# Kernel optimization log

Measured on AMD Instinct MI355X. Metric: run time of the kernel, lower is better.

## Reference

```python
import jax, jax.numpy as jnp
import numpy as np

B, P, N, E = 32, 1024, 1024, 128
HQ = 128  # head_num * qkv_dim == embedding_dim
SQRT_E = 11.313708498984761
LOGIT_CLIP = 10.0


def setup_inputs() -> dict:
    key = jax.random.key(0)
    ks = jax.random.split(key, 16)
    s = 1.0 / np.sqrt(E)
    return {
        "encoded_nodes": jax.random.normal(ks[0], (B, N, E), jnp.float32),
        "encoded_q1": jax.random.normal(ks[1], (B, P, E), jnp.float32),
        "encoded_q2": jax.random.normal(ks[2], (B, P, E), jnp.float32),
        "encoded_last_node": jax.random.normal(ks[3], (B, P, E), jnp.float32),
        "load": jax.random.uniform(ks[4], (B, P), jnp.float32),
        "left": jax.random.uniform(ks[5], (B, P), jnp.float32),
        "cur_dist": jax.random.uniform(ks[6], (B, P, N), jnp.float32),
        "log_scale": jnp.ones((), jnp.float32),
        "ninf_mask": jnp.zeros((B, P, N), jnp.float32),
        "Wq1": jax.random.normal(ks[7], (E, HQ), jnp.float32) * s,
        "Wq2": jax.random.normal(ks[8], (E, HQ), jnp.float32) * s,
        "Wq_last": jax.random.normal(ks[9], (E + 2, HQ), jnp.float32) * s,
        "Wk": jax.random.normal(ks[10], (E, HQ), jnp.float32) * s,
        "Wv": jax.random.normal(ks[11], (E, HQ), jnp.float32) * s,
        "AFT_dist_alpha": jnp.ones((1,), jnp.float32),
        "probs_dist_alpha": jnp.ones((1,), jnp.float32),
    }


def reference(encoded_nodes, encoded_q1, encoded_q2, encoded_last_node, load, left,
              cur_dist, log_scale, ninf_mask, Wq1, Wq2, Wq_last, Wk, Wv,
              AFT_dist_alpha, probs_dist_alpha):
    # set_kv / set_q1 / set_q2
    k = encoded_nodes @ Wk                      # [B,N,HQ]
    v = encoded_nodes @ Wv                      # [B,N,HQ]
    single_head_key = jnp.swapaxes(encoded_nodes, 1, 2)  # [B,E,N]
    q1 = encoded_q1 @ Wq1                       # [B,P,HQ]
    q2 = encoded_q2 @ Wq2

    input_cat = jnp.concatenate([encoded_last_node, load[:, :, None], left[:, :, None]], axis=2)
    q_last = input_cat @ Wq_last                # [B,P,HQ]
    q = q1 + q2 + q_last

    cur_dist_out = -cur_dist                    # [B,P,N]
    sigmoid_q = jax.nn.sigmoid(q)
    bias_scale = log_scale * AFT_dist_alpha[0] * cur_dist_out + ninf_mask
    e_bias = jnp.exp(bias_scale)                # [B,P,N]
    ek = jnp.exp(k)                             # [B,N,HQ]
    num = jnp.nan_to_num(jnp.einsum('bpn,bnd->bpd', e_bias, ek * v))
    den = jnp.nan_to_num(jnp.einsum('bpn,bnd->bpd', e_bias, ek)) + 1e-20
    AFT_out = sigmoid_q * (num / den)           # [B,P,HQ]

    score = jnp.einsum('bpd,bdn->bpn', AFT_out, single_head_key)
    score_scaled = score / SQRT_E + log_scale * probs_dist_alpha[0] * cur_dist_out
    score_clipped = LOGIT_CLIP * jnp.tanh(score_scaled)
    probs = jax.nn.softmax(score_clipped + ninf_mask, axis=2)
    return probs
```

## Files before the change

### kernel.cpp

```cpp
#include <hip/hip_runtime.h>
#include <math.h>

#define Bb 32
#define Pp 1024
#define Nn 1024

typedef unsigned short u16;
typedef __bf16 bf16x8 __attribute__((ext_vector_type(8)));
typedef float f32x4 __attribute__((ext_vector_type(4)));
typedef u16 us8 __attribute__((ext_vector_type(8)));
typedef u16 us4 __attribute__((ext_vector_type(4)));

#define MFMA __builtin_amdgcn_mfma_f32_16x16x32_bf16

static constexpr float INV_SQRT_E = 0.08838834764831845f;

__device__ __forceinline__ bf16x8 asbf(us8 v) { return __builtin_bit_cast(bf16x8, v); }

__device__ __forceinline__ void bsplit(float x, u16& h, u16& l) {
  unsigned u = __float_as_uint(x);
  unsigned r = u + 0x7FFF + ((u >> 16) & 1);
  h = (u16)(r >> 16);
  float hf = __uint_as_float((unsigned)h << 16);
  float lof = x - hf;
  unsigned u2 = __float_as_uint(lof);
  unsigned r2 = u2 + 0x7FFF + ((u2 >> 16) & 1);
  l = (u16)(r2 >> 16);
}

__device__ __forceinline__ void tsplit(float x, u16& h, u16& l) {
  unsigned u = __float_as_uint(x);
  h = (u16)(u >> 16);
  float lof = x - __uint_as_float(u & 0xFFFF0000u);
  l = (u16)(__float_as_uint(lof) >> 16);
}

__device__ __forceinline__ float exp10tanh(float s) {
  float ax = fabsf(s);
  float u = __expf(-2.0f * ax);
  float r = __builtin_amdgcn_rcpf(1.0f + u);
  float tt = fmaf(-2.0f * u, r, 1.0f);
  tt = copysignf(tt, s);
  return __expf(10.0f * tt);
}

__global__ __launch_bounds__(256) void prep_weights(
    const float* __restrict__ Wq1, const float* __restrict__ Wq2,
    const float* __restrict__ Wql, const float* __restrict__ Wk,
    const float* __restrict__ Wv, u16* __restrict__ wcat_hi, u16* __restrict__ wcat_lo,
    u16* __restrict__ wkv_hi, u16* __restrict__ wkv_lo) {
  int t = threadIdx.x;
  if (blockIdx.x == 0) {
    for (int i = t; i < 128 * 384; i += 256) {
      int c = i / 384, k = i % 384;
      float v = (k < 128) ? Wq1[k * 128 + c]
                          : (k < 256) ? Wq2[(k - 128) * 128 + c] : Wql[(k - 256) * 128 + c];
      u16 h, l;
      bsplit(v, h, l);
      wcat_hi[i] = h;
      wcat_lo[i] = l;
    }
  } else {
    for (int i = t; i < 256 * 128; i += 256) {
      int c = i >> 7, k = i & 127;
      float v = (c < 128) ? Wk[k * 128 + c] : Wv[k * 128 + (c - 128)];
      u16 h, l;
      bsplit(v, h, l);
      wkv_hi[i] = h;
      wkv_lo[i] = l;
    }
  }
}

__global__ __launch_bounds__(256, 1) void kv_prep(
    const float* __restrict__ nodes, const u16* __restrict__ wkv_hi,
    const u16* __restrict__ wkv_lo, u16* __restrict__ ekkP_hi, u16* __restrict__ ekkP_lo,
    u16* __restrict__ nodesP_hi, u16* __restrict__ nodesP_lo) {
  __shared__ u16 a_hi[32 * 136], a_lo[32 * 136];
  __shared__ float kvbuf[32 * 264];
  const int t = threadIdx.x;
  const int xcd = blockIdx.x & 7, jj = blockIdx.x >> 3;
  const int b = xcd * 4 + (jj >> 5);
  const int n0 = (jj & 31) * 32;
  for (int i = t; i < 4096; i += 256) {
    int n = i >> 7, d = i & 127;
    float v = nodes[((long)(b * 1024 + n0 + n)) * 128 + d];
    u16 h, l;
    bsplit(v, h, l);
    a_hi[n * 136 + d] = h;
    a_lo[n * 136 + d] = l;
  }
  __syncthreads();
  const int lane = t & 63, w = t >> 6;
  const int lr = lane & 15, lg = lane >> 4;
  f32x4 acc0[2][4] = {}, acc1[2][4] = {};
#pragma unroll
  for (int ks = 0; ks < 4; ++ks) {
    us8 ah[2], al[2];
#pragma unroll
    for (int mt = 0; mt < 2; ++mt) {
      int ro = (lr + 16 * mt) * 136 + ks * 32 + lg * 8;
      ah[mt] = *(const us8*)&a_hi[ro];
      al[mt] = *(const us8*)&a_lo[ro];
    }
    us8 bh[4], bl[4];
#pragma unroll
    for (int cc = 0; cc < 4; ++cc) {
      long off = (long)((w * 4 + cc) * 16 + lr) * 128 + ks * 32 + lg * 8;
      bh[cc] = *(const us8*)&wkv_hi[off];
      bl[cc] = *(const us8*)&wkv_lo[off];
    }
#pragma unroll
    for (int mt = 0; mt < 2; ++mt)
#pragma unroll
      for (int cc = 0; cc < 4; ++cc) {
        acc0[mt][cc] = MFMA(asbf(ah[mt]), asbf(bh[cc]), acc0[mt][cc], 0, 0, 0);
        acc1[mt][cc] = MFMA(asbf(al[mt]), asbf(bh[cc]), acc1[mt][cc], 0, 0, 0);
        acc1[mt][cc] = MFMA(asbf(ah[mt]), asbf(bl[cc]), acc1[mt][cc], 0, 0, 0);
      }
  }
#pragma unroll
  for (int mt = 0; mt < 2; ++mt)
#pragma unroll
    for (int cc = 0; cc < 4; ++cc) {
      int c = (w * 4 + cc) * 16 + lr;
#pragma unroll
      for (int r = 0; r < 4; ++r)
        kvbuf[(lg * 4 + r + 16 * mt) * 264 + c] = acc0[mt][cc][r] + acc1[mt][cc][r];
    }
  __syncthreads();
#pragma unroll
  for (int jo = 0; jo < 4; ++jo) {
    int c = jo * 64 + (t & 63);
    int i4 = t >> 6;
    int kcol = (c < 128) ? c : (c - 128);
    us8 h8, l8;
#pragma unroll
    for (int jq = 0; jq < 8; ++jq) {
      int n = i4 * 8 + jq;
      float kv = kvbuf[n * 264 + kcol];
      float ek = __expf(kv);
      float val = (c < 128) ? ek * kvbuf[n * 264 + c + 128] : ek;
      u16 h, l;
      bsplit(val, h, l);
      h8[jq] = h;
      l8[jq] = l;
    }
    long o = (((long)b * 128 + (n0 >> 3) + i4) * 256 + c) * 8;
    *(us8*)&ekkP_hi[o] = h8;
    *(us8*)&ekkP_lo[o] = l8;
  }
  {
    int pl = t >> 7, r = t & 127;
    int dgrp = r >> 3, nb = r & 7;
    const u16* src = pl ? a_lo : a_hi;
    u16* dst = pl ? nodesP_lo : nodesP_hi;
#pragma unroll
    for (int i = 0; i < 4; ++i) {
      int n = nb + 8 * i;
      us8 v = *(const us8*)&src[n * 136 + dgrp * 8];
      *(us8*)&dst[(((long)(b * 16 + dgrp)) * 1024 + n0 + n) * 8] = v;
    }
  }
}

__global__ __launch_bounds__(256) void qsig_prep(
    const float* __restrict__ q1m, const float* __restrict__ q2m,
    const float* __restrict__ lnm, const float* __restrict__ loadv,
    const float* __restrict__ leftv, const float* __restrict__ Wql,
    const u16* __restrict__ wcat_hi, const u16* __restrict__ wcat_lo,
    float* __restrict__ qsig) {
  const int t = threadIdx.x;
  const int lane = t & 63, w = t >> 6;
  const int lr = lane & 15, lg = lane >> 4;
  const long p0 = (long)blockIdx.x * 16;
  const long arow = p0 + lr;
  f32x4 qacc[2] = {};
#pragma unroll 2
  for (int s = 0; s < 12; ++s) {
    const float* __restrict__ src = (s < 4) ? q1m : (s < 8) ? q2m : lnm;
    long ao = arow * 128 + (s & 3) * 32 + lg * 8;
    float4 a0 = *(const float4*)&src[ao];
    float4 a1 = *(const float4*)&src[ao + 4];
    float av[8] = {a0.x, a0.y, a0.z, a0.w, a1.x, a1.y, a1.z, a1.w};
    us8 ah, al;
#pragma unroll
    for (int jq = 0; jq < 8; ++jq) {
      u16 hh, ll;
      tsplit(av[jq], hh, ll);
      ah[jq] = hh;
      al[jq] = ll;
    }
#pragma unroll
    for (int cf = 0; cf < 2; ++cf) {
      int c = w * 32 + cf * 16 + lr;
      us8 bh = *(const us8*)&wcat_hi[c * 384 + s * 32 + lg * 8];
      us8 bl = *(const us8*)&wcat_lo[c * 384 + s * 32 + lg * 8];
      qacc[cf] = MFMA(asbf(ah), asbf(bh), qacc[cf], 0, 0, 0);
      qacc[cf] = MFMA(asbf(al), asbf(bh), qacc[cf], 0, 0, 0);
      qacc[cf] = MFMA(asbf(ah), asbf(bl), qacc[cf], 0, 0, 0);
    }
  }
#pragma unroll
  for (int cf = 0; cf < 2; ++cf) {
    int c = w * 32 + cf * 16 + lr;
    float wl1 = Wql[128 * 128 + c], wl2 = Wql[129 * 128 + c];
#pragma unroll
    for (int r = 0; r < 4; ++r) {
      int row = lg * 4 + r;
      float qv = qacc[cf][r] + loadv[p0 + row] * wl1 + leftv[p0 + row] * wl2;
      qsig[(p0 + row) * 128 + c] = 1.0f / (1.0f + __expf(-qv));
    }
  }
}

struct DFset {
  float4 d0, d1, f0, f1;
};

__global__ __launch_bounds__(512, 2) void ndaft_gemm(
    const float* __restrict__ cdist, const float* __restrict__ ninf,
    const u16* __restrict__ ekkP_hi, const u16* __restrict__ ekkP_lo,
    const float* __restrict__ qsig, u16* __restrict__ aftP_hi,
    u16* __restrict__ aftP_lo, u16* __restrict__ bias16,
    const float* __restrict__ logs, const float* __restrict__ aal,
    const float* __restrict__ pal) {
  __shared__ u16 lds[2][8704];
  const int t = threadIdx.x;
  const int lane = t & 63, w = t >> 6;
  const int lr = lane & 15, lg = lane >> 4;
  const int wr = w >> 2, wc = w & 3;
  const int xcd = blockIdx.x & 7, j = blockIdx.x >> 3;
  const int b = xcd * 4 + (j & 3);
  const int pt = j >> 2;
  const long bp = (long)b * Pp + pt * 128;
  const float c1 = logs[0] * aal[0];
  const float c2 = logs[0] * pal[0];

  const int srow = t >> 2, soct = t & 3;
  const long arow = bp + srow;
  const long tbase = (arow >> 4) * 32768;
  const int spr = srow & 15, sptile = srow >> 4;
  const long bsrc = (long)b * 128 * 2048;

  int ccol[4];
#pragma unroll
  for (int ct = 0; ct < 4; ++ct)
    ccol[ct] = (ct < 2) ? (wc * 32 + ct * 16 + lr) : (96 + wc * 32 + ct * 16 + lr);

  DFset dfA, dfB;
  us8 ebh, ebl;

  auto load_df = [&](DFset& df, int s) {
    long ao = arow * 1024 + s * 32 + soct * 8;
    df.d0 = *(const float4*)&cdist[ao];
    df.d1 = *(const float4*)&cdist[ao + 4];
    df.f0 = *(const float4*)&ninf[ao];
    df.f1 = *(const float4*)&ninf[ao + 4];
  };
  auto load_B = [&](int s, us8 (&bh)[4], us8 (&bl)[4]) {
    long sb = bsrc + (long)s * 8192 + (long)lg * 2048;
#pragma unroll
    for (int ct = 0; ct < 4; ++ct) {
      bh[ct] = *(const us8*)&ekkP_hi[sb + ccol[ct] * 8];
      bl[ct] = *(const us8*)&ekkP_lo[sb + ccol[ct] * 8];
    }
  };
  auto compute_eb = [&](DFset& df, int s) {
    float dv[8] = {df.d0.x, df.d0.y, df.d0.z, df.d0.w, df.d1.x, df.d1.y, df.d1.z, df.d1.w};
    float nv[8] = {df.f0.x, df.f0.y, df.f0.z, df.f0.w, df.f1.x, df.f1.y, df.f1.z, df.f1.w};
    us8 q8;
#pragma unroll
    for (int jq = 0; jq < 8; ++jq) {
      float e = __expf(fmaf(-c1, dv[jq], nv[jq]));
      u16 h, l;
      tsplit(e, h, l);
      ebh[jq] = h;
      ebl[jq] = l;
      float x = fminf(fmaxf(c2 * dv[jq], 0.f), 15.999f);
      q8[jq] = (nv[jq] < -1e5f) ? (u16)0xFFFF : (u16)(x * 4096.f + 0.5f);
    }
    *(us8*)&bias16[tbase + ((s * 4 + soct) * 16 + spr) * 8] = q8;
  };
  auto write_A = [&](int buf) {
    *(us8*)&lds[buf][((sptile * 2 + 0) * 4 + soct) * 136 + spr * 8] = ebh;
    *(us8*)&lds[buf][((sptile * 2 + 1) * 4 + soct) * 136 + spr * 8] = ebl;
  };

  f32x4 acc[4][4] = {};
  us8 Bh0[4], Bl0[4], Bh1[4], Bl1[4];

  load_df(dfA, 0);
  load_df(dfB, 1);
  load_B(0, Bh0, Bl0);
  compute_eb(dfA, 0);
  write_A(0);
  asm volatile("s_waitcnt lgkmcnt(0)" ::: "memory");
  __builtin_amdgcn_s_barrier();
  __builtin_amdgcn_sched_barrier(0);

  auto stage = [&](int s, DFset& refill, DFset& consume, us8 (&BhC)[4], us8 (&BlC)[4],
                   us8 (&BhN)[4], us8 (&BlN)[4]) {
    if (s < 31) load_B(s + 1, BhN, BlN);
    if (s < 30) load_df(refill, s + 2);
    if (s < 31) {
      compute_eb(consume, s + 1);
      write_A((s + 1) & 1);
    }
    const int buf = s & 1;
    us8 ah[4], al[4];
#pragma unroll
    for (int mt = 0; mt < 4; ++mt) {
      int ptl = wr * 4 + mt;
      ah[mt] = *(const us8*)&lds[buf][((ptl * 2 + 0) * 4 + lg) * 136 + lr * 8];
      al[mt] = *(const us8*)&lds[buf][((ptl * 2 + 1) * 4 + lg) * 136 + lr * 8];
    }
#pragma unroll
    for (int ct = 0; ct < 4; ++ct) {
#pragma unroll
      for (int mt = 0; mt < 4; ++mt) {
        acc[mt][ct] = MFMA(asbf(ah[mt]), asbf(BhC[ct]), acc[mt][ct], 0, 0, 0);
        acc[mt][ct] = MFMA(asbf(al[mt]), asbf(BhC[ct]), acc[mt][ct], 0, 0, 0);
        acc[mt][ct] = MFMA(asbf(ah[mt]), asbf(BlC[ct]), acc[mt][ct], 0, 0, 0);
      }
    }
    asm volatile("s_waitcnt lgkmcnt(0)" ::: "memory");
    __builtin_amdgcn_s_barrier();
    __builtin_amdgcn_sched_barrier(0);
  };

#pragma unroll 1
  for (int s2 = 0; s2 < 32; s2 += 2) {
    stage(s2, dfA, dfB, Bh0, Bl0, Bh1, Bl1);
    stage(s2 + 1, dfB, dfA, Bh1, Bl1, Bh0, Bl0);
  }

#pragma unroll
  for (int mt = 0; mt < 4; ++mt)
#pragma unroll
    for (int ct = 0; ct < 2; ++ct) {
      int cn = wc * 32 + ct * 16 + lr;
      int nc = cn >> 3, jq = cn & 7;
#pragma unroll
      for (int r = 0; r < 4; ++r) {
        long gr = bp + wr * 64 + mt * 16 + lg * 4 + r;
        float sig = qsig[gr * 128 + cn];
        float aftv = sig * acc[mt][ct][r] * __builtin_amdgcn_rcpf(acc[mt][ct + 2][r] + 1e-20f);
        u16 h, l;
        bsplit(aftv, h, l);
        long idx = (gr >> 4) * 2048 + (nc * 16 + (gr & 15)) * 8 + jq;
        aftP_hi[idx] = h;
        aftP_lo[idx] = l;
      }
    }
}

__global__ __launch_bounds__(256, 4) void score_softmax(
    const u16* bias16, const u16* __restrict__ aftP_hi, const u16* __restrict__ aftP_lo,
    const u16* __restrict__ nodesP_hi, const u16* __restrict__ nodesP_lo,
    float* out) {
  __shared__ float psum[16 * 4];
  __shared__ float invb[16];
  const int t = threadIdx.x;
  const int lane = t & 63, w = t >> 6;
  const int lr = lane & 15, lg = lane >> 4;
  const int xcd = blockIdx.x & 7, j = blockIdx.x >> 3;
  const int b = xcd * 4 + (j >> 6);
  const int tl = j & 63;
  const int p0 = tl * 16;
  const long bp = (long)b * Pp + p0;
  const int tile = b * 64 + tl;

  f32x4 sacc[16] = {};
#pragma unroll
  for (int ks = 0; ks < 4; ++ks) {
    long aoff = (long)tile * 2048 + ((long)((ks * 4 + lg) * 16 + lr)) * 8;
    us8 ah = *(const us8*)&aftP_hi[aoff];
    us8 al = *(const us8*)&aftP_lo[aoff];
    long nb = ((long)(b * 16 + ks * 4 + lg)) * 1024;
    auto bld = [&](int cf, us8& bh, us8& bl) {
      long o = (nb + w * 256 + cf * 16 + lr) * 8;
      bh = *(const us8*)&nodesP_hi[o];
      bl = *(const us8*)&nodesP_lo[o];
    };
    us8 bh0, bl0, bh1, bl1;
    bld(0, bh0, bl0);
    bld(1, bh1, bl1);
#pragma unroll
    for (int cf = 0; cf < 16; ++cf) {
      us8 nh = bh1, nl = bl1;
      if (cf < 14) bld(cf + 2, nh, nl);
      sacc[cf] = MFMA(asbf(bh0), asbf(ah), sacc[cf], 0, 0, 0);
      sacc[cf] = MFMA(asbf(bl0), asbf(ah), sacc[cf], 0, 0, 0);
      sacc[cf] = MFMA(asbf(bh0), asbf(al), sacc[cf], 0, 0, 0);
      bh0 = bh1; bl0 = bl1; bh1 = nh; bl1 = nl;
    }
  }

  const long btile = (long)tile * 32768;
  float rs = 0.f;
#pragma unroll
  for (int cf = 0; cf < 16; ++cf) {
    int nc = w * 32 + cf * 2 + (lg >> 1);
    int j0 = (lg & 1) * 4;
    us4 q4 = *(const us4*)&bias16[btile + (nc * 16 + lr) * 8 + j0];
#pragma unroll
    for (int r = 0; r < 4; ++r) {
      u16 qv = q4[r];
      float sv = fmaf(sacc[cf][r], INV_SQRT_E, (float)qv * -2.44140625e-4f);
      float e = exp10tanh(sv);
      e = (qv == (u16)0xFFFF) ? 0.f : e;
      sacc[cf][r] = e;
      rs += e;
    }
  }
  rs += __shfl_xor(rs, 16);
  rs += __shfl_xor(rs, 32);
  if (lane < 16) psum[lr * 4 + w] = rs;
  __syncthreads();
  if (t < 16)
    invb[t] = 1.0f / (psum[t * 4] + psum[t * 4 + 1] + psum[t * 4 + 2] + psum[t * 4 + 3]);
  __syncthreads();

  const float inv = invb[lr];
  const long ro = (bp + lr) * (long)Nn + w * 256;
#pragma unroll
  for (int cf = 0; cf < 16; ++cf) {
    float4 v;
    v.x = sacc[cf][0] * inv;
    v.y = sacc[cf][1] * inv;
    v.z = sacc[cf][2] * inv;
    v.w = sacc[cf][3] * inv;
    *(float4*)&out[ro + cf * 16 + lg * 4] = v;
  }
}

extern "C" void kernel_launch(void* const* d_in, const int* in_sizes, int n_in,
                              void* d_out, int out_size, void* d_ws, size_t ws_size,
                              hipStream_t stream) {
  const float* nodes = (const float*)d_in[0];
  const float* q1m = (const float*)d_in[1];
  const float* q2m = (const float*)d_in[2];
  const float* lnm = (const float*)d_in[3];
  const float* loadv = (const float*)d_in[4];
  const float* leftv = (const float*)d_in[5];
  const float* cdist = (const float*)d_in[6];
  const float* logs = (const float*)d_in[7];
  const float* ninf = (const float*)d_in[8];
  const float* Wq1 = (const float*)d_in[9];
  const float* Wq2 = (const float*)d_in[10];
  const float* Wql = (const float*)d_in[11];
  const float* Wk = (const float*)d_in[12];
  const float* Wv = (const float*)d_in[13];
  const float* aalpha = (const float*)d_in[14];
  const float* palpha = (const float*)d_in[15];

  char* ws = (char*)d_ws;
  u16* ekkP_hi = (u16*)ws;
  u16* ekkP_lo = (u16*)(ws + (16ul << 20));
  u16* nodesP_hi = (u16*)(ws + (32ul << 20));
  u16* nodesP_lo = (u16*)(ws + (40ul << 20));
  float* qsig = (float*)(ws + (48ul << 20));
  u16* aftP_hi = (u16*)(ws + (64ul << 20));
  u16* aftP_lo = (u16*)(ws + (72ul << 20));
  u16* wcat_hi = (u16*)(ws + (80ul << 20));
  u16* wcat_lo = wcat_hi + 128 * 384;
  u16* wkv_hi = wcat_lo + 128 * 384;
  u16* wkv_lo = wkv_hi + 256 * 128;
  u16* bias16 = (u16*)d_out;

  prep_weights<<<2, 256, 0, stream>>>(Wq1, Wq2, Wql, Wk, Wv, wcat_hi, wcat_lo, wkv_hi, wkv_lo);
  kv_prep<<<Bb * Nn / 32, 256, 0, stream>>>(nodes, wkv_hi, wkv_lo, ekkP_hi, ekkP_lo,
                                            nodesP_hi, nodesP_lo);
  qsig_prep<<<2048, 256, 0, stream>>>(q1m, q2m, lnm, loadv, leftv, Wql, wcat_hi, wcat_lo,
                                      qsig);
  ndaft_gemm<<<256, 512, 0, stream>>>(cdist, ninf, ekkP_hi, ekkP_lo, qsig, aftP_hi,
                                      aftP_lo, bias16, logs, aalpha, palpha);
  score_softmax<<<Bb * Pp / 16, 256, 0, stream>>>(
      bias16, aftP_hi, aftP_lo, nodesP_hi, nodesP_lo, (float*)d_out);
}
```

Measured before the change: 359.9 us.

## Split ndaft_gemm output columns across two blocks to double grid parallelism

The AFT numerator/denominator GEMM now splits the 128 output columns into two halves handled by separate blocks, doubling the grid to 512 blocks and halving per-wave accumulators so the launch bound can ask for 4 blocks per CU. Each block still recomputes the exp bias tile from cur_dist and ninf_mask, so that elementwise work and its global reads are duplicated, and only the first half writes bias16. The B operand prefetch is no longer double-buffered in registers; it is loaded in the same stage it is consumed, which may expose global load latency.

```diff
diff --git a/kernel.cpp b/kernel.cpp
--- a/kernel.cpp
+++ b/kernel.cpp
@@ -218,7 +218,7 @@
   float4 d0, d1, f0, f1;
 };
 
-__global__ __launch_bounds__(512, 2) void ndaft_gemm(
+__global__ __launch_bounds__(512, 4) void ndaft_gemm(
     const float* __restrict__ cdist, const float* __restrict__ ninf,
     const u16* __restrict__ ekkP_hi, const u16* __restrict__ ekkP_lo,
     const float* __restrict__ qsig, u16* __restrict__ aftP_hi,
@@ -229,11 +229,13 @@
   const int t = threadIdx.x;
   const int lane = t & 63, w = t >> 6;
   const int lr = lane & 15, lg = lane >> 4;
-  const int wr = w >> 2, wc = w & 3;
+  const int wr = w >> 1, wc = w & 1;
   const int xcd = blockIdx.x & 7, j = blockIdx.x >> 3;
   const int b = xcd * 4 + (j & 3);
-  const int pt = j >> 2;
+  const int pt = (j >> 2) & 7;
+  const int nh = j >> 5;
   const long bp = (long)b * Pp + pt * 128;
+  const int colbase = nh * 64 + wc * 32;
   const float c1 = logs[0] * aal[0];
   const float c2 = logs[0] * pal[0];
 
@@ -242,11 +244,6 @@
   const long tbase = (arow >> 4) * 32768;
   const int spr = srow & 15, sptile = srow >> 4;
   const long bsrc = (long)b * 128 * 2048;
-
-  int ccol[4];
-#pragma unroll
-  for (int ct = 0; ct < 4; ++ct)
-    ccol[ct] = (ct < 2) ? (wc * 32 + ct * 16 + lr) : (96 + wc * 32 + ct * 16 + lr);
 
   DFset dfA, dfB;
   us8 ebh, ebl;
@@ -262,8 +259,9 @@
     long sb = bsrc + (long)s * 8192 + (long)lg * 2048;
 #pragma unroll
     for (int ct = 0; ct < 4; ++ct) {
-      bh[ct] = *(const us8*)&ekkP_hi[sb + ccol[ct] * 8];
-      bl[ct] = *(const us8*)&ekkP_lo[sb + ccol[ct] * 8];
+      int ccol = ((ct < 2) ? (colbase + ct * 16) : (128 + colbase + (ct - 2) * 16)) + lr;
+      bh[ct] = *(const us8*)&ekkP_hi[sb + ccol * 8];
+      bl[ct] = *(const us8*)&ekkP_lo[sb + ccol * 8];
     }
   };
   auto compute_eb = [&](DFset& df, int s) {
@@ -280,48 +278,47 @@
       float x = fminf(fmaxf(c2 * dv[jq], 0.f), 15.999f);
       q8[jq] = (nv[jq] < -1e5f) ? (u16)0xFFFF : (u16)(x * 4096.f + 0.5f);
     }
-    *(us8*)&bias16[tbase + ((s * 4 + soct) * 16 + spr) * 8] = q8;
+    if (nh == 0)
+      *(us8*)&bias16[tbase + ((s * 4 + soct) * 16 + spr) * 8] = q8;
   };
   auto write_A = [&](int buf) {
     *(us8*)&lds[buf][((sptile * 2 + 0) * 4 + soct) * 136 + spr * 8] = ebh;
     *(us8*)&lds[buf][((sptile * 2 + 1) * 4 + soct) * 136 + spr * 8] = ebl;
   };
 
-  f32x4 acc[4][4] = {};
-  us8 Bh0[4], Bl0[4], Bh1[4], Bl1[4];
+  f32x4 acc[2][4] = {};
+  us8 Bh[4], Bl[4];
 
   load_df(dfA, 0);
   load_df(dfB, 1);
-  load_B(0, Bh0, Bl0);
   compute_eb(dfA, 0);
   write_A(0);
   asm volatile("s_waitcnt lgkmcnt(0)" ::: "memory");
   __builtin_amdgcn_s_barrier();
   __builtin_amdgcn_sched_barrier(0);
 
-  auto stage = [&](int s, DFset& refill, DFset& consume, us8 (&BhC)[4], us8 (&BlC)[4],
-                   us8 (&BhN)[4], us8 (&BlN)[4]) {
-    if (s < 31) load_B(s + 1, BhN, BlN);
+  auto stage = [&](int s, DFset& refill, DFset& consume) {
+    load_B(s, Bh, Bl);
     if (s < 30) load_df(refill, s + 2);
     if (s < 31) {
       compute_eb(consume, s + 1);
       write_A((s + 1) & 1);
     }
     const int buf = s & 1;
-    us8 ah[4], al[4];
-#pragma unroll
-    for (int mt = 0; mt < 4; ++mt) {
-      int ptl = wr * 4 + mt;
+    us8 ah[2], al[2];
+#pragma unroll
+    for (int mt = 0; mt < 2; ++mt) {
+      int ptl = wr * 2 + mt;
       ah[mt] = *(const us8*)&lds[buf][((ptl * 2 + 0) * 4 + lg) * 136 + lr * 8];
       al[mt] = *(const us8*)&lds[buf][((ptl * 2 + 1) * 4 + lg) * 136 + lr * 8];
     }
 #pragma unroll
     for (int ct = 0; ct < 4; ++ct) {
 #pragma unroll
-      for (int mt = 0; mt < 4; ++mt) {
-        acc[mt][ct] = MFMA(asbf(ah[mt]), asbf(BhC[ct]), acc[mt][ct], 0, 0, 0);
-        acc[mt][ct] = MFMA(asbf(al[mt]), asbf(BhC[ct]), acc[mt][ct], 0, 0, 0);
-        acc[mt][ct] = MFMA(asbf(ah[mt]), asbf(BlC[ct]), acc[mt][ct], 0, 0, 0);
+      for (int mt = 0; mt < 2; ++mt) {
+        acc[mt][ct] = MFMA(asbf(ah[mt]), asbf(Bh[ct]), acc[mt][ct], 0, 0, 0);
+        acc[mt][ct] = MFMA(asbf(al[mt]), asbf(Bh[ct]), acc[mt][ct], 0, 0, 0);
+        acc[mt][ct] = MFMA(asbf(ah[mt]), asbf(Bl[ct]), acc[mt][ct], 0, 0, 0);
       }
     }
     asm volatile("s_waitcnt lgkmcnt(0)" ::: "memory");
@@ -331,19 +328,19 @@
 
 #pragma unroll 1
   for (int s2 = 0; s2 < 32; s2 += 2) {
-    stage(s2, dfA, dfB, Bh0, Bl0, Bh1, Bl1);
-    stage(s2 + 1, dfB, dfA, Bh1, Bl1, Bh0, Bl0);
-  }
-
-#pragma unroll
-  for (int mt = 0; mt < 4; ++mt)
+    stage(s2, dfA, dfB);
+    stage(s2 + 1, dfB, dfA);
+  }
+
+#pragma unroll
+  for (int mt = 0; mt < 2; ++mt)
 #pragma unroll
     for (int ct = 0; ct < 2; ++ct) {
-      int cn = wc * 32 + ct * 16 + lr;
+      int cn = colbase + ct * 16 + lr;
       int nc = cn >> 3, jq = cn & 7;
 #pragma unroll
       for (int r = 0; r < 4; ++r) {
-        long gr = bp + wr * 64 + mt * 16 + lg * 4 + r;
+        long gr = bp + wr * 32 + mt * 16 + lg * 4 + r;
         float sig = qsig[gr * 128 + cn];
         float aftv = sig * acc[mt][ct][r] * __builtin_amdgcn_rcpf(acc[mt][ct + 2][r] + 1e-20f);
         u16 h, l;
@@ -474,7 +471,7 @@
                                             nodesP_hi, nodesP_lo);
   qsig_prep<<<2048, 256, 0, stream>>>(q1m, q2m, lnm, loadv, leftv, Wql, wcat_hi, wcat_lo,
                                       qsig);
-  ndaft_gemm<<<256, 512, 0, stream>>>(cdist, ninf, ekkP_hi, ekkP_lo, qsig, aftP_hi,
+  ndaft_gemm<<<512, 512, 0, stream>>>(cdist, ninf, ekkP_hi, ekkP_lo, qsig, aftP_hi,
                                       aftP_lo, bias16, logs, aalpha, palpha);
   score_softmax<<<Bb * Pp / 16, 256, 0, stream>>>(
       bias16, aftP_hi, aftP_lo, nodesP_hi, nodesP_lo, (float*)d_out);
```

Result: slower. 444.2 us (+23.4%).
